# Optimization experiments

Hardware: AMD Instinct MI355X
Metric: run time of the kernel (lower is better)

Reference implementation:

```python
import jax, jax.numpy as jnp
import numpy as np

HEAD_DIM = 128  # head_dim passed to the hook; num_heads = hidden // HEAD_DIM


def _matmul_hadU(y):
    """Walsh-Hadamard butterfly over last axis, exactly mirroring matmul_hadU
    (K == 1, power-of-two n). y: (B, n) -> (B, n), scaled by 1/sqrt(n)."""
    B, n = y.shape
    y = y[..., None]  # (B, n, 1), mirrors X.view(-1, n, 1)
    while y.shape[1] > 1:
        m, c = y.shape[1] // 2, y.shape[2]
        y = y.reshape(B, m, 2, c)
        a, b = y[:, :, 0, :], y[:, :, 1, :]
        # out[:,:,0,:] = a+b ; out[:,:,1,:] = a-b ; then flatten last two dims
        y = jnp.stack([a + b, a - b], axis=2).reshape(B, m, 2 * c)
    return y.reshape(B, n) * (1.0 / np.sqrt(n)).astype(np.float32)


def setup_inputs() -> dict:
    key = jax.random.key(0)
    x = jax.random.normal(key, (4, 4096, 4096), dtype=jnp.float32)
    return {"x": x}


def reference(x):
    init_shape = x.shape
    hidden = init_shape[-1]
    num_heads = hidden // HEAD_DIM  # 32
    # (*, hidden) -> (T, num_heads, head_dim) -> (T, head_dim, num_heads)
    xt = x.reshape(-1, num_heads, HEAD_DIM).transpose(0, 2, 1)
    T = xt.shape[0]
    # Hadamard on the num_heads (last) axis
    y = _matmul_hadU(xt.reshape(T * HEAD_DIM, num_heads)).reshape(T, HEAD_DIM, num_heads)
    # transpose back and restore original shape
    return y.transpose(0, 2, 1).reshape(init_shape)
```

## Files before the change

kernel.cpp:

```cpp
#include <hip/hip_runtime.h>


#define NUM_HEADS 32
#define ROW_F4 1024
#define HEAD_F4 32

__global__ __launch_bounds__(256) void fwht_heads_kernel(
    const float* __restrict__ x, float* __restrict__ out, int num_rows) {
    int tid = blockIdx.x * blockDim.x + threadIdx.x;
    int d4 = tid & 31;
    long long row = tid >> 5;
    if (row >= num_rows) return;

    const float4* __restrict__ xp = (const float4*)x + row * ROW_F4 + d4;
    float4* __restrict__ op = (float4*)out + row * ROW_F4 + d4;

    float4 v[NUM_HEADS];
#pragma unroll
    for (int h = 0; h < NUM_HEADS; ++h) {
        v[h] = xp[h * HEAD_F4];
    }

#pragma unroll
    for (int s = 1; s < NUM_HEADS; s <<= 1) {
#pragma unroll
        for (int i = 0; i < NUM_HEADS; ++i) {
            if ((i & s) == 0) {
                int j = i | s;
                float4 a = v[i];
                float4 b = v[j];
                v[i] = make_float4(a.x + b.x, a.y + b.y, a.z + b.z, a.w + b.w);
                v[j] = make_float4(a.x - b.x, a.y - b.y, a.z - b.z, a.w - b.w);
            }
        }
    }

    const float scale = 0.17677669529663687f;
#pragma unroll
    for (int h = 0; h < NUM_HEADS; ++h) {
        float4 a = v[h];
        op[h * HEAD_F4] =
            make_float4(a.x * scale, a.y * scale, a.z * scale, a.w * scale);
    }
}

extern "C" void kernel_launch(void* const* d_in, const int* in_sizes, int n_in,
                              void* d_out, int out_size, void* d_ws, size_t ws_size,
                              hipStream_t stream) {
    const float* x = (const float*)d_in[0];
    float* out = (float*)d_out;

    int total = in_sizes[0];
    int num_rows = total / 4096;
    int threads = num_rows * 32;

    dim3 block(256);
    dim3 grid((threads + 255) / 256);
    fwht_heads_kernel<<<grid, block, 0, stream>>>(x, out, num_rows);
}
```

Before: 428.4 us.

## Split 32-point head Hadamard across 4 lanes using in-register shuffles

Each row's 32-head Hadamard transform is now spread across 4 threads. Every thread holds 8 heads, runs a local 8-point butterfly, and finishes the last two stages with xor-shuffles and sign flips. This cuts per-thread register use from 128 floats to 32 and quadruples the thread count, which should raise occupancy and memory-level parallelism on a bandwidth-bound kernel. The cost is extra cross-lane shuffle instructions, and lanes that share a head are now interleaved differently, which changes the coalescing pattern.

```diff
diff --git a/kernel.cpp b/kernel.cpp
--- a/kernel.cpp
+++ b/kernel.cpp
@@ -1,60 +1,76 @@
 #include <hip/hip_runtime.h>
 
 
-#define NUM_HEADS 32
-#define ROW_F4 1024
-#define HEAD_F4 32
+__global__ __launch_bounds__(256) void fwht_heads_shfl(
+    const float4* __restrict__ x, float4* __restrict__ out, int total_threads) {
+    int t = blockIdx.x * blockDim.x + threadIdx.x;
+    if (t >= total_threads) return;
+    int row = t >> 7;
+    int r = t & 127;
+    int j = r & 3;
+    int d4 = r >> 2;
 
-__global__ __launch_bounds__(256) void fwht_heads_kernel(
-    const float* __restrict__ x, float* __restrict__ out, int num_rows) {
-    int tid = blockIdx.x * blockDim.x + threadIdx.x;
-    int d4 = tid & 31;
-    long long row = tid >> 5;
-    if (row >= num_rows) return;
+    int base = row * 1024 + j * 32 + d4;
+    const float4* __restrict__ xp = x + base;
 
-    const float4* __restrict__ xp = (const float4*)x + row * ROW_F4 + d4;
-    float4* __restrict__ op = (float4*)out + row * ROW_F4 + d4;
-
-    float4 v[NUM_HEADS];
+    float4 v[8];
 #pragma unroll
-    for (int h = 0; h < NUM_HEADS; ++h) {
-        v[h] = xp[h * HEAD_F4];
-    }
+    for (int k = 0; k < 8; ++k) v[k] = xp[k * 128];
 
 #pragma unroll
-    for (int s = 1; s < NUM_HEADS; s <<= 1) {
+    for (int s = 1; s < 8; s <<= 1) {
 #pragma unroll
-        for (int i = 0; i < NUM_HEADS; ++i) {
-            if ((i & s) == 0) {
-                int j = i | s;
-                float4 a = v[i];
-                float4 b = v[j];
-                v[i] = make_float4(a.x + b.x, a.y + b.y, a.z + b.z, a.w + b.w);
-                v[j] = make_float4(a.x - b.x, a.y - b.y, a.z - b.z, a.w - b.w);
+        for (int k = 0; k < 8; ++k) {
+            if ((k & s) == 0) {
+                int m = k | s;
+                float4 a = v[k], b = v[m];
+                v[k] = make_float4(a.x + b.x, a.y + b.y, a.z + b.z, a.w + b.w);
+                v[m] = make_float4(a.x - b.x, a.y - b.y, a.z - b.z, a.w - b.w);
             }
         }
     }
 
+    float sg1 = (j & 1) ? -1.0f : 1.0f;
+    float sg2 = (j & 2) ? -1.0f : 1.0f;
+#pragma unroll
+    for (int k = 0; k < 8; ++k) {
+        float4 o = v[k];
+        float4 p;
+        p.x = __shfl_xor(o.x, 1);
+        p.y = __shfl_xor(o.y, 1);
+        p.z = __shfl_xor(o.z, 1);
+        p.w = __shfl_xor(o.w, 1);
+        o = make_float4(sg1 * o.x + p.x, sg1 * o.y + p.y,
+                        sg1 * o.z + p.z, sg1 * o.w + p.w);
+        p.x = __shfl_xor(o.x, 2);
+        p.y = __shfl_xor(o.y, 2);
+        p.z = __shfl_xor(o.z, 2);
+        p.w = __shfl_xor(o.w, 2);
+        v[k] = make_float4(sg2 * o.x + p.x, sg2 * o.y + p.y,
+                           sg2 * o.z + p.z, sg2 * o.w + p.w);
+    }
+
     const float scale = 0.17677669529663687f;
+    float4* __restrict__ op = out + base;
 #pragma unroll
-    for (int h = 0; h < NUM_HEADS; ++h) {
-        float4 a = v[h];
-        op[h * HEAD_F4] =
-            make_float4(a.x * scale, a.y * scale, a.z * scale, a.w * scale);
+    for (int k = 0; k < 8; ++k) {
+        float4 a = v[k];
+        op[k * 128] = make_float4(a.x * scale, a.y * scale,
+                                  a.z * scale, a.w * scale);
     }
 }
 
 extern "C" void kernel_launch(void* const* d_in, const int* in_sizes, int n_in,
                               void* d_out, int out_size, void* d_ws, size_t ws_size,
                               hipStream_t stream) {
-    const float* x = (const float*)d_in[0];
-    float* out = (float*)d_out;
+    const float4* x = (const float4*)d_in[0];
+    float4* out = (float4*)d_out;
 
     int total = in_sizes[0];
     int num_rows = total / 4096;
-    int threads = num_rows * 32;
+    int total_threads = num_rows * 128;
 
     dim3 block(256);
-    dim3 grid((threads + 255) / 256);
-    fwht_heads_kernel<<<grid, block, 0, stream>>>(x, out, num_rows);
+    dim3 grid((total_threads + 255) / 256);
+    fwht_heads_shfl<<<grid, block, 0, stream>>>(x, out, total_threads);
 }
```

Result: no change. 426.9 us (-0.3%).
